# Optimization experiments

Hardware: AMD Instinct MI355X
Metric: run time of the kernel (lower is better)

## Reference

```python
import jax, jax.numpy as jnp
import numpy as np

N_NODES = 100000
N_EDGES = 3200000
IN_DIM = 16
HID = 64


def setup_inputs() -> dict:
    key = jax.random.key(0)
    k_x, k_e, k_w1, k_w2 = jax.random.split(key, 4)
    x = jax.random.normal(k_x, (N_NODES, IN_DIM), dtype=jnp.float32)
    edge_index = jax.random.randint(k_e, (2, N_EDGES), 0, N_NODES, dtype=jnp.int64)
    # PyTorch Linear default init: U(-1/sqrt(fan_in), 1/sqrt(fan_in)); use scaled normal analog
    W1 = jax.random.normal(k_w1, (2 * IN_DIM, HID), dtype=jnp.float32) / np.sqrt(2 * IN_DIM)
    b1 = jnp.zeros((HID,), dtype=jnp.float32)
    W2 = jax.random.normal(k_w2, (HID, 1), dtype=jnp.float32) / np.sqrt(HID)
    b2 = jnp.zeros((1,), dtype=jnp.float32)
    return {"x": x, "edge_index": edge_index, "W1": W1, "b1": b1, "W2": W2, "b2": b2}


def reference(x, edge_index, W1, b1, W2, b2):
    row = edge_index[0]
    col = edge_index[1]
    bi = x[col]                      # [E, IN_DIM] gather of receiver features
    bo = x[row]                      # [E, IN_DIM] gather of sender features
    B = jnp.concatenate([bi, bo], axis=-1)  # [E, 2*IN_DIM]
    h = jnp.tanh(B @ W1 + b1)        # [E, HID]
    return jax.nn.sigmoid(h @ W2 + b2)  # [E, 1]
```

## Files before the change

kernel.cpp:

```cpp
#include <hip/hip_runtime.h>


typedef __attribute__((ext_vector_type(8)))  short bf16x8;
typedef __attribute__((ext_vector_type(4)))  float f32x4;
typedef __attribute__((ext_vector_type(16))) float f32x16;
typedef __attribute__((ext_vector_type(4)))  unsigned short u16x4;

#define LOG2E 1.4426950408889634f

__device__ __forceinline__ float asm_exp2(float x) {
    float r;
    asm("v_exp_f32 %0, %1" : "=v"(r) : "v"(x));
    return r;
}
__device__ __forceinline__ float asm_rcp(float x) {
    float r;
    asm("v_rcp_f32 %0, %1" : "=v"(r) : "v"(x));
    return r;
}

template <bool B> struct BC { static constexpr bool value = B; };

__device__ __forceinline__ unsigned short f2bf(float f) {
    unsigned u = __float_as_uint(f);
    u += 0x7fffu + ((u >> 16) & 1u);
    return (unsigned short)(u >> 16);
}

__global__ void prep(const float* __restrict__ x, unsigned short* __restrict__ xb, int n,
                     const unsigned* __restrict__ ei, int* __restrict__ flag) {
    if (blockIdx.x == 0 && threadIdx.x < 64) {
        unsigned v = ei[2 * threadIdx.x + 1];
        unsigned long long nz = __ballot(v != 0u);
        if (threadIdx.x == 0) flag[0] = (nz == 0ull) ? 1 : 0;
    }
    int i = (blockIdx.x * blockDim.x + threadIdx.x) * 4;
    if (i >= n) return;
    f32x4 v = *(const f32x4*)(x + i);
    u16x4 o;
    o[0] = f2bf(v[0]); o[1] = f2bf(v[1]); o[2] = f2bf(v[2]); o[3] = f2bf(v[3]);
    *(u16x4*)(xb + i) = o;
}

__global__ void detect_idx64(const unsigned* __restrict__ ei, int* __restrict__ flag) {
    unsigned v = ei[2 * threadIdx.x + 1];
    unsigned long long nz = __ballot(v != 0u);
    if (threadIdx.x == 0) flag[0] = (nz == 0ull) ? 1 : 0;
}

struct IdxPair { int c, r; };

template <bool USE_XB, bool EXACT>
__global__ void __launch_bounds__(256)
edge_mlp(const void* __restrict__ ei,
         const float* __restrict__ x,
         const unsigned short* __restrict__ xb,
         const float* __restrict__ W1,
         const float* __restrict__ b1,
         const float* __restrict__ W2,
         const float* __restrict__ b2,
         float* __restrict__ out,
         const int* __restrict__ flag,
         int E, int ntiles)
{
    __shared__ float2 tbl[64];

    const int lane = threadIdx.x & 63;
    const int l31  = lane & 31;
    const int g    = lane >> 5;
    const int gwave  = blockIdx.x * (blockDim.x >> 6) + (threadIdx.x >> 6);
    const int nwaves = gridDim.x * (blockDim.x >> 6);

    const int idx64 = flag ? flag[0] : 0;
    const float S = 2.0f * LOG2E;

    {
        int tid = threadIdx.x;
        if (tid < 64) {
            int tg = tid >> 5, tb = (tid >> 4) & 1, tj = tid & 15;
            int rowv = (tj & 3) + 8 * (tj >> 2) + 4 * tg;
            int h = 32 * tb + rowv;
            float2 cw;
            cw.x = exp2f(S * b1[h]);
            cw.y = -2.0f * W2[h];
            tbl[tid] = cw;
        }
    }

    bf16x8 w1f00, w1f01, w1f10, w1f11;
    {
        union { bf16x8 v; unsigned short u[8]; } t00, t01, t10, t11;
#pragma unroll
        for (int b = 0; b < 8; ++b) {
            int k0 = 8 * g + b;
            t00.u[b] = f2bf(S * W1[(k0)      * 64 + l31]);
            t01.u[b] = f2bf(S * W1[(16 + k0) * 64 + l31]);
            t10.u[b] = f2bf(S * W1[(k0)      * 64 + 32 + l31]);
            t11.u[b] = f2bf(S * W1[(16 + k0) * 64 + 32 + l31]);
        }
        w1f00 = t00.v; w1f01 = t01.v; w1f10 = t10.v; w1f11 = t11.v;
    }

    float pbase = 0.f;
#pragma unroll
    for (int j = 0; j < 16; ++j) {
        int rowv = (j & 3) + 8 * (j >> 2) + 4 * g;
        pbase += W2[rowv] + W2[32 + rowv];
    }
    const float bias2 = b2[0];

    __syncthreads();
    const float2* tb = &tbl[g * 32];

    const char* xbb  = (const char*)xb;
    const char* outb = (char*)out;
    const unsigned g16 = (unsigned)g << 4;

    auto body = [&](auto bc) {
        constexpr bool IDX64 = decltype(bc)::value;
        const unsigned sh = IDX64 ? 3u : 2u;
        const char* eiR = (const char*)ei;
        const char* eiC = (const char*)ei + ((size_t)E << sh);

        auto load_idx = [&](int tt) -> IdxPair {
            int e = tt * 32 + l31;
            unsigned ec;
            if (EXACT) ec = (unsigned)e;
            else       ec = (unsigned)(e < E ? e : E - 1);
            unsigned off = ec << sh;
            IdxPair ip;
            ip.r = *(const int*)(eiR + off);
            ip.c = *(const int*)(eiC + off);
            return ip;
        };
        auto gather = [&](int node) -> bf16x8 {
            if (USE_XB) {
                unsigned off = ((unsigned)node << 5) + g16;
                return *(const bf16x8*)(xbb + off);
            } else {
                const float* px = x + (size_t)node * 16 + 8 * g;
                f32x4 v0 = *(const f32x4*)px;
                f32x4 v1 = *(const f32x4*)(px + 4);
                union { bf16x8 v; unsigned short u[8]; } t;
#pragma unroll
                for (int b = 0; b < 4; ++b) { t.u[b] = f2bf(v0[b]); t.u[b + 4] = f2bf(v1[b]); }
                return t.v;
            }
        };

        int t = gwave;
        if (t >= ntiles) return;
        IdxPair ic = load_idx(t);
        bf16x8 fc = gather(ic.c);
        bf16x8 fr = gather(ic.r);
        int tn = t + nwaves;
        IdxPair inx = load_idx(tn < ntiles ? tn : ntiles - 1);

        const f32x16 ZC = 0.0f;

        while (true) {
            bf16x8 fcn = gather(inx.c);
            bf16x8 frn = gather(inx.r);
            int tnn = tn + nwaves;
            IdxPair inn = load_idx(tnn < ntiles ? tnn : ntiles - 1);

            f32x16 acc0 = __builtin_amdgcn_mfma_f32_32x32x16_bf16(w1f00, fc, ZC, 0, 0, 0);
            acc0        = __builtin_amdgcn_mfma_f32_32x32x16_bf16(w1f01, fr, acc0, 0, 0, 0);
            f32x16 acc1 = __builtin_amdgcn_mfma_f32_32x32x16_bf16(w1f10, fc, ZC, 0, 0, 0);
            acc1        = __builtin_amdgcn_mfma_f32_32x32x16_bf16(w1f11, fr, acc1, 0, 0, 0);

            float p0 = pbase, p1 = 0.f, p2 = 0.f, p3 = 0.f;
#pragma unroll
            for (int j = 0; j < 16; ++j) {
                float2 cw = tb[j];
                float e  = asm_exp2(acc0[j]);
                float rv = asm_rcp(fmaf(cw.x, e, 1.0f));
                float pj = fmaf(cw.y, rv, (j & 3) == 0 ? p0 : (j & 3) == 1 ? p1 : (j & 3) == 2 ? p2 : p3);
                if      ((j & 3) == 0) p0 = pj;
                else if ((j & 3) == 1) p1 = pj;
                else if ((j & 3) == 2) p2 = pj;
                else                   p3 = pj;
            }
#pragma unroll
            for (int j = 0; j < 16; ++j) {
                float2 cw = tb[16 + j];
                float e  = asm_exp2(acc1[j]);
                float rv = asm_rcp(fmaf(cw.x, e, 1.0f));
                float pj = fmaf(cw.y, rv, (j & 3) == 0 ? p0 : (j & 3) == 1 ? p1 : (j & 3) == 2 ? p2 : p3);
                if      ((j & 3) == 0) p0 = pj;
                else if ((j & 3) == 1) p1 = pj;
                else if ((j & 3) == 2) p2 = pj;
                else                   p3 = pj;
            }
            float p = (p0 + p1) + (p2 + p3);
            p += __shfl_xor(p, 32);
            float z = p + bias2;
            float res = asm_rcp(1.0f + asm_exp2(-z * LOG2E));

            unsigned eoff = ((unsigned)(t * 32 + l31)) << 2;
            if (EXACT) {
                if (lane < 32) *(float*)(outb + eoff) = res;
            } else {
                if (lane < 32 && (t * 32 + l31) < E) *(float*)(outb + eoff) = res;
            }

            if (tn >= ntiles) break;
            t = tn; tn = tnn;
            inx = inn; fc = fcn; fr = frn;
        }
    };

    if (idx64) body(BC<true>{});
    else       body(BC<false>{});
}

extern "C" void kernel_launch(void* const* d_in, const int* in_sizes, int n_in,
                              void* d_out, int out_size, void* d_ws, size_t ws_size,
                              hipStream_t stream)
{
    const float* x  = (const float*)d_in[0];
    const void*  ei = d_in[1];
    const float* W1 = (const float*)d_in[2];
    const float* b1 = (const float*)d_in[3];
    const float* W2 = (const float*)d_in[4];
    const float* b2 = (const float*)d_in[5];
    float* out = (float*)d_out;

    const int E      = in_sizes[1] / 2;
    const int nx     = in_sizes[0];
    const int ntiles = (E + 31) / 32;
    const bool exact = (E % 32) == 0;

    int* flag = nullptr;
    unsigned short* xb = nullptr;
    bool use_xb = false;
    if (ws_size >= 4) flag = (int*)d_ws;
    if (ws_size >= 256 + (size_t)nx * 2) {
        xb = (unsigned short*)((char*)d_ws + 256);
        use_xb = true;
    }

    if (use_xb) {
        int nth = (nx + 3) / 4;
        prep<<<(nth + 255) / 256, 256, 0, stream>>>(x, xb, nx, (const unsigned*)ei, flag);
    } else if (flag) {
        detect_idx64<<<1, 64, 0, stream>>>((const unsigned*)ei, flag);
    }

    const int blocks = 2048;
    if (use_xb) {
        if (exact) edge_mlp<true , true ><<<blocks, 256, 0, stream>>>(ei, x, xb, W1, b1, W2, b2, out, flag, E, ntiles);
        else       edge_mlp<true , false><<<blocks, 256, 0, stream>>>(ei, x, xb, W1, b1, W2, b2, out, flag, E, ntiles);
    } else {
        if (exact) edge_mlp<false, true ><<<blocks, 256, 0, stream>>>(ei, x, xb, W1, b1, W2, b2, out, flag, E, ntiles);
        else       edge_mlp<false, false><<<blocks, 256, 0, stream>>>(ei, x, xb, W1, b1, W2, b2, out, flag, E, ntiles);
    }
}
```

Measured before the change: 62.93 us.

## Combine four sigmoid-weighted terms under one reciprocal and retune grid size

Rewrites the per-element epilogue so that four terms of the form c_y/(1+c_x*e) are summed as a single fraction: the denominators are multiplied together and only one v_rcp is issued per group of four instead of four. This cuts transcendental (rcp) instructions by 4x at the cost of extra multiplies and FMAs. The table is now read with float4 loads. The grid drops from 2048 to 1250 blocks, clamped to the tile count, which changes how many tiles each wave processes. The product of four denominators risks overflow to inf when the exp terms are large, which could yield NaN for saturated tanh units.

```diff
diff --git a/kernel.cpp b/kernel.cpp
--- a/kernel.cpp
+++ b/kernel.cpp
@@ -110,7 +110,7 @@
     const float bias2 = b2[0];
 
     __syncthreads();
-    const float2* tb = &tbl[g * 32];
+    const float4* t4 = (const float4*)(&tbl[g * 32]);
 
     const char* xbb  = (const char*)xb;
     const char* outb = (char*)out;
@@ -169,30 +169,29 @@
             f32x16 acc1 = __builtin_amdgcn_mfma_f32_32x32x16_bf16(w1f10, fc, ZC, 0, 0, 0);
             acc1        = __builtin_amdgcn_mfma_f32_32x32x16_bf16(w1f11, fr, acc1, 0, 0, 0);
 
-            float p0 = pbase, p1 = 0.f, p2 = 0.f, p3 = 0.f;
-#pragma unroll
-            for (int j = 0; j < 16; ++j) {
-                float2 cw = tb[j];
-                float e  = asm_exp2(acc0[j]);
-                float rv = asm_rcp(fmaf(cw.x, e, 1.0f));
-                float pj = fmaf(cw.y, rv, (j & 3) == 0 ? p0 : (j & 3) == 1 ? p1 : (j & 3) == 2 ? p2 : p3);
-                if      ((j & 3) == 0) p0 = pj;
-                else if ((j & 3) == 1) p1 = pj;
-                else if ((j & 3) == 2) p2 = pj;
-                else                   p3 = pj;
+            float p = pbase;
+#pragma unroll
+            for (int q = 0; q < 8; ++q) {
+                const f32x16& A = (q < 4) ? acc0 : acc1;
+                int k = (q & 3) * 4;
+                float4 c01 = t4[2 * q];
+                float4 c23 = t4[2 * q + 1];
+                float E0 = asm_exp2(A[k]);
+                float E1 = asm_exp2(A[k + 1]);
+                float E2 = asm_exp2(A[k + 2]);
+                float E3 = asm_exp2(A[k + 3]);
+                float D0 = fmaf(c01.x, E0, 1.0f);
+                float D1 = fmaf(c01.z, E1, 1.0f);
+                float D2 = fmaf(c23.x, E2, 1.0f);
+                float D3 = fmaf(c23.z, E3, 1.0f);
+                float D01 = D0 * D1;
+                float D23 = D2 * D3;
+                float N01 = fmaf(c01.y, D1, c01.w * D0);
+                float N23 = fmaf(c23.y, D3, c23.w * D2);
+                float N   = fmaf(N01, D23, N23 * D01);
+                float P   = D01 * D23;
+                p = fmaf(N, asm_rcp(P), p);
             }
-#pragma unroll
-            for (int j = 0; j < 16; ++j) {
-                float2 cw = tb[16 + j];
-                float e  = asm_exp2(acc1[j]);
-                float rv = asm_rcp(fmaf(cw.x, e, 1.0f));
-                float pj = fmaf(cw.y, rv, (j & 3) == 0 ? p0 : (j & 3) == 1 ? p1 : (j & 3) == 2 ? p2 : p3);
-                if      ((j & 3) == 0) p0 = pj;
-                else if ((j & 3) == 1) p1 = pj;
-                else if ((j & 3) == 2) p2 = pj;
-                else                   p3 = pj;
-            }
-            float p = (p0 + p1) + (p2 + p3);
             p += __shfl_xor(p, 32);
             float z = p + bias2;
             float res = asm_rcp(1.0f + asm_exp2(-z * LOG2E));
@@ -247,7 +246,8 @@
         detect_idx64<<<1, 64, 0, stream>>>((const unsigned*)ei, flag);
     }
 
-    const int blocks = 2048;
+    int blocks = 1250;
+    if (ntiles < blocks * 4) blocks = (ntiles + 3) / 4;
     if (use_xb) {
         if (exact) edge_mlp<true , true ><<<blocks, 256, 0, stream>>>(ei, x, xb, W1, b1, W2, b2, out, flag, E, ntiles);
         else       edge_mlp<true , false><<<blocks, 256, 0, stream>>>(ei, x, xb, W1, b1, W2, b2, out, flag, E, ntiles);
```

Measured after the change: 62.64 us. Within noise of the previous version (-0.5%).
